# Optimization experiments

Measured on AMD Instinct MI355X. Metric: run time of the kernel, lower is better.

Reference implementation:

```python
import jax, jax.numpy as jnp
import numpy as np

N_NODES = 100000
N_EDGES = 1600000
F_IN = 128
HID = 128
N_LAYERS = 4
N_CLASSES = 10
N_GRAPHS = 512
BN_EPS = 1e-5


def setup_inputs() -> dict:
    key = jax.random.key(0)
    ks = jax.random.split(key, 16)
    x = jax.random.normal(ks[0], (N_NODES, F_IN), dtype=jnp.float32)
    edge_index = jax.random.randint(ks[1], (2, N_EDGES), 0, N_NODES, dtype=jnp.int64)
    edge_attr = jax.random.normal(ks[2], (N_EDGES, 8), dtype=jnp.float32)
    batch = jnp.sort(jax.random.randint(ks[3], (N_NODES,), 0, N_GRAPHS, dtype=jnp.int64))
    # Per-layer MLP params (in-dim is 128 for all layers since F_IN == HID).
    s1 = 1.0 / np.sqrt(F_IN)
    s2 = 1.0 / np.sqrt(2 * HID)
    W1 = jax.random.uniform(ks[4], (N_LAYERS, F_IN, 2 * HID), minval=-s1, maxval=s1, dtype=jnp.float32)
    b1 = jax.random.uniform(ks[5], (N_LAYERS, 2 * HID), minval=-s1, maxval=s1, dtype=jnp.float32)
    gamma1 = jnp.ones((N_LAYERS, 2 * HID), dtype=jnp.float32)
    beta1 = jnp.zeros((N_LAYERS, 2 * HID), dtype=jnp.float32)
    W2 = jax.random.uniform(ks[6], (N_LAYERS, 2 * HID, HID), minval=-s2, maxval=s2, dtype=jnp.float32)
    b2 = jax.random.uniform(ks[7], (N_LAYERS, HID), minval=-s2, maxval=s2, dtype=jnp.float32)
    sf = 1.0 / np.sqrt(HID * N_LAYERS)
    fcW = jax.random.uniform(ks[8], (HID * N_LAYERS, N_CLASSES), minval=-sf, maxval=sf, dtype=jnp.float32)
    fcb = jax.random.uniform(ks[9], (N_CLASSES,), minval=-sf, maxval=sf, dtype=jnp.float32)
    return {"x": x, "edge_index": edge_index, "edge_attr": edge_attr, "batch": batch,
            "W1": W1, "b1": b1, "gamma1": gamma1, "beta1": beta1,
            "W2": W2, "b2": b2, "fcW": fcW, "fcb": fcb}


def reference(x, edge_index, edge_attr, batch, W1, b1, gamma1, beta1, W2, b2, fcW, fcb):
    # edge_attr is unused by the original forward.
    src, dst = edge_index[0], edge_index[1]
    n = x.shape[0]
    # In-degree for mean aggregation (messages flow src -> dst in PyG).
    deg = jax.ops.segment_sum(jnp.ones((src.shape[0],), x.dtype), dst, num_segments=n)
    inv_deg = 1.0 / jnp.maximum(deg, 1.0)
    h = x
    xs = []
    for i in range(N_LAYERS):
        # GINConv, eps=0, aggr='mean': nn(x + mean_j h_j)
        agg = jax.ops.segment_sum(h[src], dst, num_segments=n) * inv_deg[:, None]
        z = h + agg
        z = z @ W1[i] + b1[i]                      # [N, 2H]
        mu = jnp.mean(z, axis=0)
        var = jnp.mean(jnp.square(z - mu), axis=0)  # biased var (BN training mode)
        z = gamma1[i] * (z - mu) * jax.lax.rsqrt(var + BN_EPS) + beta1[i]
        z = jax.nn.relu(z)
        z = z @ W2[i] + b2[i]                      # [N, H]
        h = jax.nn.relu(z)
        xs.append(h)
    xcat = jnp.concatenate(xs, axis=1)             # [N, H*L]
    # global_mean_pool over graph ids
    gsum = jax.ops.segment_sum(xcat, batch, num_segments=N_GRAPHS)
    gcnt = jax.ops.segment_sum(jnp.ones((n,), xcat.dtype), batch, num_segments=N_GRAPHS)
    pooled = gsum / jnp.maximum(gcnt, 1.0)[:, None]
    logits = pooled @ fcW + fcb
    return jax.nn.log_softmax(logits, axis=-1)
```

## Files before the change

kernel.cpp:

```cpp
#include <hip/hip_runtime.h>
#include <cstdint>
#include <cstddef>

#define NN 100000
#define NE 1600000
#define FD 128
#define HD2 256
#define NLAYERS 4
#define NGR 512
#define NCLS 10
#define BNEPS 1e-5f
#define G1TILES 1563
#define GEMM_GRID 521
#define EB 6250
#define NB 391
#define NSLICE 8
#define SLICEW 12500

typedef unsigned short ushort_t;
typedef short bf16x8 __attribute__((ext_vector_type(8)));
typedef float f32x4 __attribute__((ext_vector_type(4)));

__device__ __forceinline__ float bfl(unsigned short u) {
  unsigned v = ((unsigned)u) << 16;
  return __builtin_bit_cast(float, v);
}
__device__ __forceinline__ unsigned short fbf(float f) {
  unsigned u = __builtin_bit_cast(unsigned, f);
  unsigned r = (u + 0x7FFFu + ((u >> 16) & 1u)) >> 16;
  return (unsigned short)r;
}

__global__ void k_init_detect(const int* ei, int* flag, int* degi) {
  int i = blockIdx.x * 256 + threadIdx.x;
  if (i < NN) degi[i] = 0;
  if (blockIdx.x == 0) {
    __shared__ int nz;
    if (threadIdx.x == 0) nz = 0;
    __syncthreads();
    if (ei[2 * threadIdx.x + 1] != 0) atomicAdd(&nz, 1);
    __syncthreads();
    if (threadIdx.x == 0) flag[0] = (nz == 0) ? 1 : 0;
  }
}

__global__ void k_repack(const int* ei, const int* batch, const int* flag,
                         int* src32, int* dst32, int* batch32) {
  int i = blockIdx.x * 256 + threadIdx.x;
  const bool wide = (flag[0] != 0);
  if (i < NE) {
    src32[i] = wide ? ei[2 * i] : ei[i];
    dst32[i] = wide ? ei[2 * (NE + i)] : ei[NE + i];
  }
  if (i < NN) batch32[i] = wide ? batch[2 * i] : batch[i];
}

__global__ void k_deg8(const int* __restrict__ dst, int* degi) {
  int slice = blockIdx.x & (NSLICE - 1);
  int e = (blockIdx.x >> 3) * 256 + threadIdx.x;
  if (e >= NE) return;
  int d = dst[e];
  int lo = slice * SLICEW;
  if (d >= lo && d < lo + SLICEW) atomicAdd(&degi[d], 1);
}

__global__ void k_scan1(const int* degi, int* rowptr, int* bsum) {
  __shared__ int s[256];
  int t = threadIdx.x;
  int i = blockIdx.x * 256 + t;
  int v = (i < NN) ? degi[i] : 0;
  s[t] = v;
  __syncthreads();
  for (int off = 1; off < 256; off <<= 1) {
    int x = (t >= off) ? s[t - off] : 0;
    __syncthreads();
    s[t] += x;
    __syncthreads();
  }
  if (i < NN) rowptr[i] = s[t] - v;
  if (t == 255) bsum[blockIdx.x] = s[255];
}

__global__ void k_scan2_gstats(int* bsum, int nb, const int* __restrict__ batch,
                               int* __restrict__ gstart, int* __restrict__ gcnti) {
  __shared__ int s[512];
  int t = threadIdx.x;
  int v = (t < nb) ? bsum[t] : 0;
  s[t] = v;
  __syncthreads();
  for (int off = 1; off < 512; off <<= 1) {
    int x = (t >= off) ? s[t - off] : 0;
    __syncthreads();
    s[t] += x;
    __syncthreads();
  }
  if (t < nb) bsum[t] = s[t] - v;
  if (t < NGR) {
    int g = t;
    int lo = 0, hi = NN;
    while (lo < hi) { int m = (lo + hi) >> 1; if (batch[m] < g) lo = m + 1; else hi = m; }
    int st = lo;
    hi = NN;
    while (lo < hi) { int m = (lo + hi) >> 1; if (batch[m] < g + 1) lo = m + 1; else hi = m; }
    gstart[g] = st;
    gcnti[g] = lo - st;
  }
}

__global__ void k_scan3_cursor(int* rowptr, const int* bsum, int* cursor,
                               const int* degi, float* inv_deg) {
  int i = blockIdx.x * 256 + threadIdx.x;
  if (i < NN) {
    int r = rowptr[i] + bsum[blockIdx.x];
    rowptr[i] = r;
    cursor[i] = r;
    inv_deg[i] = 1.f / fmaxf((float)degi[i], 1.f);
  }
  if (i == 0) rowptr[NN] = NE;
}

__global__ void k_scatter8(const int* __restrict__ src, const int* __restrict__ dst,
                           int* cursor, int* csr) {
  int slice = blockIdx.x & (NSLICE - 1);
  int e = (blockIdx.x >> 3) * 256 + threadIdx.x;
  if (e >= NE) return;
  int d = dst[e];
  int lo = slice * SLICEW;
  if (d >= lo && d < lo + SLICEW) {
    int p = atomicAdd(&cursor[d], 1);
    csr[p] = src[e];
  }
}

__global__ void k_cvt_x(const float* __restrict__ x, ushort_t* __restrict__ xb) {
  int i = blockIdx.x * 256 + threadIdx.x;
  if (i >= NN * FD / 8) return;
  const float4* p = (const float4*)x + (size_t)i * 2;
  float4 a = p[0], b = p[1];
  bf16x8 o;
  o[0] = (short)fbf(a.x); o[1] = (short)fbf(a.y);
  o[2] = (short)fbf(a.z); o[3] = (short)fbf(a.w);
  o[4] = (short)fbf(b.x); o[5] = (short)fbf(b.y);
  o[6] = (short)fbf(b.z); o[7] = (short)fbf(b.w);
  *(bf16x8*)&xb[(size_t)i * 8] = o;
}

__global__ void k_cvt_w(const float* __restrict__ W1, const float* __restrict__ W2,
                        ushort_t* __restrict__ W1t, ushort_t* __restrict__ W2t) {
  int idx = blockIdx.x * 256 + threadIdx.x;
  if (idx >= NLAYERS * FD * HD2) return;
  int l = idx >> 15, r = idx & 32767;
  {
    int n = r >> 7, k = r & 127;
    W1t[(size_t)l * 32768 + n * 128 + k] = fbf(W1[(size_t)l * 32768 + k * 256 + n]);
  }
  {
    int n = r >> 8, k = r & 255;
    W2t[(size_t)l * 32768 + n * 256 + k] = fbf(W2[(size_t)l * 32768 + k * 128 + n]);
  }
}

__global__ void k_agg(const ushort_t* __restrict__ h, const int* __restrict__ rowptr,
                      const int* __restrict__ csr, const float* __restrict__ inv_deg,
                      ushort_t* __restrict__ tout, float* bnsum) {
  if (blockIdx.x == 0) {
    bnsum[threadIdx.x] = 0.f;
    bnsum[HD2 + threadIdx.x] = 0.f;
  }
  const int wave = threadIdx.x >> 6;
  const int lane = threadIdx.x & 63;
  const int q = lane >> 4, sub = lane & 15;
  const int node = blockIdx.x * 16 + wave * 4 + q;
  const uint4* h16 = (const uint4*)h;
  int beg = rowptr[node];
  int deg = rowptr[node + 1] - beg;
  int m1 = max(deg, __shfl_xor(deg, 16));
  int maxd = max(m1, __shfl_xor(m1, 32));
  float a0 = 0.f, a1 = 0.f, a2 = 0.f, a3 = 0.f;
  float a4 = 0.f, a5 = 0.f, a6 = 0.f, a7 = 0.f;
  int j = 0;
  for (; j + 8 <= maxd; j += 8) {
    uint4 p[8];
#pragma unroll
    for (int u = 0; u < 8; ++u) {
      bool valid = (j + u) < deg;
      int idx = beg + (valid ? j + u : 0);
      int s = csr[idx];
      uint4 v = h16[(size_t)s * 16 + sub];
      p[u].x = valid ? v.x : 0u;
      p[u].y = valid ? v.y : 0u;
      p[u].z = valid ? v.z : 0u;
      p[u].w = valid ? v.w : 0u;
    }
#pragma unroll
    for (int u = 0; u < 8; ++u) {
      a0 += bfl((unsigned short)(p[u].x & 0xFFFF));
      a1 += bfl((unsigned short)(p[u].x >> 16));
      a2 += bfl((unsigned short)(p[u].y & 0xFFFF));
      a3 += bfl((unsigned short)(p[u].y >> 16));
      a4 += bfl((unsigned short)(p[u].z & 0xFFFF));
      a5 += bfl((unsigned short)(p[u].z >> 16));
      a6 += bfl((unsigned short)(p[u].w & 0xFFFF));
      a7 += bfl((unsigned short)(p[u].w >> 16));
    }
  }
  for (; j < maxd; ++j) {
    bool valid = j < deg;
    int idx = beg + (valid ? j : 0);
    int s = csr[idx];
    uint4 v = h16[(size_t)s * 16 + sub];
    if (valid) {
      a0 += bfl((unsigned short)(v.x & 0xFFFF));
      a1 += bfl((unsigned short)(v.x >> 16));
      a2 += bfl((unsigned short)(v.y & 0xFFFF));
      a3 += bfl((unsigned short)(v.y >> 16));
      a4 += bfl((unsigned short)(v.z & 0xFFFF));
      a5 += bfl((unsigned short)(v.z >> 16));
      a6 += bfl((unsigned short)(v.w & 0xFFFF));
      a7 += bfl((unsigned short)(v.w >> 16));
    }
  }
  float id = inv_deg[node];
  uint4 c = h16[(size_t)node * 16 + sub];
  float o0 = bfl((unsigned short)(c.x & 0xFFFF)) + a0 * id;
  float o1 = bfl((unsigned short)(c.x >> 16)) + a1 * id;
  float o2 = bfl((unsigned short)(c.y & 0xFFFF)) + a2 * id;
  float o3 = bfl((unsigned short)(c.y >> 16)) + a3 * id;
  float o4 = bfl((unsigned short)(c.z & 0xFFFF)) + a4 * id;
  float o5 = bfl((unsigned short)(c.z >> 16)) + a5 * id;
  float o6 = bfl((unsigned short)(c.w & 0xFFFF)) + a6 * id;
  float o7 = bfl((unsigned short)(c.w >> 16)) + a7 * id;
  uint4 ow;
  ow.x = (unsigned)fbf(o0) | ((unsigned)fbf(o1) << 16);
  ow.y = (unsigned)fbf(o2) | ((unsigned)fbf(o3) << 16);
  ow.z = (unsigned)fbf(o4) | ((unsigned)fbf(o5) << 16);
  ow.w = (unsigned)fbf(o6) | ((unsigned)fbf(o7) << 16);
  ((uint4*)tout)[(size_t)node * 16 + sub] = ow;
}

__launch_bounds__(256, 2)
__global__ void k_gemm1(const ushort_t* __restrict__ A, const ushort_t* __restrict__ Bt,
                        const float* __restrict__ bias, ushort_t* __restrict__ Z,
                        float* __restrict__ bnsum) {
  __shared__ ushort_t Bs[256 * 128];
  __shared__ ushort_t As[64 * 128];
  const int tid = threadIdx.x;
#pragma unroll
  for (int i = 0; i < 16; ++i) {
    int chunk = tid + 256 * i;
    int n = chunk >> 4, c = chunk & 15;
    bf16x8 v = *(const bf16x8*)&Bt[n * 128 + c * 8];
    *(bf16x8*)((char*)Bs + n * 256 + ((c * 16) ^ ((n & 7) << 4))) = v;
  }
  const int wv = tid >> 6, ln = tid & 63;
  const int lr = ln & 15, lg = ln >> 4;
  float bb[16];
#pragma unroll
  for (int nt = 0; nt < 16; ++nt) bb[nt] = bias[nt * 16 + lr];
  float s0[16] = {}, s1[16] = {};

  for (int t = blockIdx.x; t < G1TILES; t += GEMM_GRID) {
    int row0 = t * 64;
#pragma unroll
    for (int i = 0; i < 4; ++i) {
      int chunk = tid + 256 * i;
      int r = chunk >> 4, c = chunk & 15;
      int grow = row0 + r; if (grow >= NN) grow = NN - 1;
      bf16x8 v = *(const bf16x8*)&A[(size_t)grow * FD + c * 8];
      *(bf16x8*)((char*)As + r * 256 + ((c * 16) ^ ((r & 7) << 4))) = v;
    }
    __syncthreads();
    int arow = wv * 16 + lr;
    bf16x8 af[4];
#pragma unroll
    for (int ks = 0; ks < 4; ++ks)
      af[ks] = *(bf16x8*)((char*)As + arow * 256 + ((ks * 64 + lg * 16) ^ ((arow & 7) << 4)));
    f32x4 acc[16];
#pragma unroll
    for (int nt = 0; nt < 16; ++nt) acc[nt] = (f32x4){0.f, 0.f, 0.f, 0.f};
#pragma unroll
    for (int nt = 0; nt < 16; ++nt) {
      int bn = nt * 16 + lr;
#pragma unroll
      for (int ks = 0; ks < 4; ++ks) {
        bf16x8 bfr = *(bf16x8*)((char*)Bs + bn * 256 + ((ks * 64 + lg * 16) ^ ((bn & 7) << 4)));
        acc[nt] = __builtin_amdgcn_mfma_f32_16x16x32_bf16(af[ks], bfr, acc[nt], 0, 0, 0);
      }
    }
    __syncthreads();
#pragma unroll
    for (int nt = 0; nt < 16; ++nt) {
      int col = nt * 16 + lr;
#pragma unroll
      for (int j = 0; j < 4; ++j) {
        int grow = row0 + wv * 16 + lg * 4 + j;
        if (grow < NN) {
          unsigned short zb = fbf(acc[nt][j] + bb[nt]);
          Z[(size_t)grow * HD2 + col] = zb;
          float zf = bfl(zb);
          s0[nt] += zf;
          s1[nt] += zf * zf;
        }
      }
    }
  }
  __syncthreads();
  float* ls = (float*)As;
  ls[tid] = 0.f; ls[tid + 256] = 0.f;
  __syncthreads();
#pragma unroll
  for (int nt = 0; nt < 16; ++nt) {
    int col = nt * 16 + lr;
    atomicAdd(&ls[col], s0[nt]);
    atomicAdd(&ls[col + 256], s1[nt]);
  }
  __syncthreads();
  if (tid < 256) {
    atomicAdd(&bnsum[tid], ls[tid]);
    atomicAdd(&bnsum[HD2 + tid], ls[tid + 256]);
  }
}

__launch_bounds__(256, 2)
__global__ void k_gemm2(const ushort_t* __restrict__ Zin, const ushort_t* __restrict__ Bt,
                        const float* __restrict__ bias, const float* __restrict__ bnsum,
                        const float* __restrict__ gamma, const float* __restrict__ beta,
                        ushort_t* __restrict__ Hout) {
  __shared__ ushort_t Bs[128 * 256];
  __shared__ ushort_t As[64 * 128];
  const int tid = threadIdx.x;
#pragma unroll
  for (int i = 0; i < 16; ++i) {
    int chunk = tid + 256 * i;
    int n = chunk >> 5, c = chunk & 31;
    bf16x8 v = *(const bf16x8*)&Bt[n * 256 + c * 8];
    *(bf16x8*)((char*)Bs + n * 512 + ((c * 16) ^ ((n & 7) << 4))) = v;
  }
  const int wv = tid >> 6, ln = tid & 63;
  const int lr = ln & 15, lg = ln >> 4;
  float a1v[2][8], a2v[2][8];
#pragma unroll
  for (int h = 0; h < 2; ++h)
#pragma unroll
    for (int j = 0; j < 8; ++j) {
      int k = h * 128 + (tid & 15) * 8 + j;
      float mu = bnsum[k] * (1.f / (float)NN);
      float var = fmaxf(bnsum[HD2 + k] * (1.f / (float)NN) - mu * mu, 0.f);
      float g = gamma[k] * rsqrtf(var + BNEPS);
      a1v[h][j] = g;
      a2v[h][j] = beta[k] - mu * g;
    }
  float bb[8];
#pragma unroll
  for (int nt = 0; nt < 8; ++nt) bb[nt] = bias[nt * 16 + lr];

  for (int t = blockIdx.x; t < G1TILES; t += GEMM_GRID) {
    int row0 = t * 64;
    f32x4 acc[8];
#pragma unroll
    for (int nt = 0; nt < 8; ++nt) acc[nt] = (f32x4){0.f, 0.f, 0.f, 0.f};
#pragma unroll
    for (int h = 0; h < 2; ++h) {
#pragma unroll
      for (int i = 0; i < 4; ++i) {
        int chunk = tid + 256 * i;
        int r = chunk >> 4, c = chunk & 15;
        int grow = row0 + r; if (grow >= NN) grow = NN - 1;
        bf16x8 v = *(const bf16x8*)&Zin[(size_t)grow * HD2 + h * 128 + c * 8];
        bf16x8 o;
#pragma unroll
        for (int j = 0; j < 8; ++j) {
          float f = bfl((unsigned short)v[j]) * a1v[h][j] + a2v[h][j];
          o[j] = (short)fbf(fmaxf(f, 0.f));
        }
        *(bf16x8*)((char*)As + r * 256 + ((c * 16) ^ ((r & 7) << 4))) = o;
      }
      __syncthreads();
      int arow = wv * 16 + lr;
      bf16x8 af[4];
#pragma unroll
      for (int ks = 0; ks < 4; ++ks)
        af[ks] = *(bf16x8*)((char*)As + arow * 256 + ((ks * 64 + lg * 16) ^ ((arow & 7) << 4)));
#pragma unroll
      for (int nt = 0; nt < 8; ++nt) {
        int bn = nt * 16 + lr;
#pragma unroll
        for (int ks = 0; ks < 4; ++ks) {
          bf16x8 bfr = *(bf16x8*)((char*)Bs + bn * 512 +
                                  (((h * 16 + ks * 4 + lg) * 16) ^ ((bn & 7) << 4)));
          acc[nt] = __builtin_amdgcn_mfma_f32_16x16x32_bf16(af[ks], bfr, acc[nt], 0, 0, 0);
        }
      }
      __syncthreads();
    }
#pragma unroll
    for (int nt = 0; nt < 8; ++nt) {
      int col = nt * 16 + lr;
#pragma unroll
      for (int j = 0; j < 4; ++j) {
        int grow = row0 + wv * 16 + lg * 4 + j;
        if (grow < NN) Hout[(size_t)grow * FD + col] = fbf(fmaxf(acc[nt][j] + bb[nt], 0.f));
      }
    }
  }
}

__launch_bounds__(256)
__global__ void k_pool_fc(const ushort_t* __restrict__ hb, const int* __restrict__ gstart,
                          const int* __restrict__ gcnti, const float* __restrict__ fcW,
                          const float* __restrict__ fcb, float* __restrict__ out) {
  __shared__ float pool4[4][512];
  __shared__ float wred[4][NCLS];
  int g = blockIdx.x, t = threadIdx.x;
  int start = gstart[g], cnt = gcnti[g];
  int chunk = t & 63, ro = t >> 6;
  int L = chunk >> 4, cc = (chunk & 15) * 8;
  const ushort_t* hL = hb + (size_t)L * NN * FD;
  float s[8] = {};
  for (int r = start + ro; r < start + cnt; r += 4) {
    bf16x8 v = *(const bf16x8*)&hL[(size_t)r * FD + cc];
#pragma unroll
    for (int j = 0; j < 8; ++j) s[j] += bfl((unsigned short)v[j]);
  }
#pragma unroll
  for (int j = 0; j < 8; ++j) pool4[ro][chunk * 8 + j] = s[j];
  __syncthreads();
  float inv = 1.f / fmaxf((float)cnt, 1.f);
  float pA = (pool4[0][t] + pool4[1][t] + pool4[2][t] + pool4[3][t]) * inv;
  float pB = (pool4[0][t + 256] + pool4[1][t + 256] + pool4[2][t + 256] + pool4[3][t + 256]) * inv;
  float pacc[NCLS];
#pragma unroll
  for (int c = 0; c < NCLS; ++c)
    pacc[c] = pA * fcW[t * NCLS + c] + pB * fcW[(t + 256) * NCLS + c];
#pragma unroll
  for (int off = 32; off > 0; off >>= 1)
#pragma unroll
    for (int c = 0; c < NCLS; ++c) pacc[c] += __shfl_down(pacc[c], off);
  if ((t & 63) == 0)
#pragma unroll
    for (int c = 0; c < NCLS; ++c) wred[t >> 6][c] = pacc[c];
  __syncthreads();
  if (t == 0) {
    float lg[NCLS];
    float mx = -1e30f;
#pragma unroll
    for (int c = 0; c < NCLS; ++c) {
      lg[c] = wred[0][c] + wred[1][c] + wred[2][c] + wred[3][c] + fcb[c];
      mx = fmaxf(mx, lg[c]);
    }
    float se = 0.f;
#pragma unroll
    for (int c = 0; c < NCLS; ++c) se += expf(lg[c] - mx);
    float lse = mx + logf(se);
#pragma unroll
    for (int c = 0; c < NCLS; ++c) out[(size_t)g * NCLS + c] = lg[c] - lse;
  }
}

extern "C" void kernel_launch(void* const* d_in, const int* in_sizes, int n_in,
                              void* d_out, int out_size, void* d_ws, size_t ws_size,
                              hipStream_t stream) {
  const float* x      = (const float*)d_in[0];
  const int*   ei     = (const int*)d_in[1];
  const int*   batch  = (const int*)d_in[3];
  const float* W1     = (const float*)d_in[4];
  const float* b1     = (const float*)d_in[5];
  const float* gamma1 = (const float*)d_in[6];
  const float* beta1  = (const float*)d_in[7];
  const float* W2     = (const float*)d_in[8];
  const float* b2     = (const float*)d_in[9];
  const float* fcW    = (const float*)d_in[10];
  const float* fcb    = (const float*)d_in[11];
  float* out = (float*)d_out;

  char* p = (char*)d_ws;
  auto alloc = [&](size_t bytes) {
    char* r = p;
    p += (bytes + 255) & ~(size_t)255;
    return r;
  };
  ushort_t* xbf   = (ushort_t*)alloc((size_t)NN * FD * 2);
  ushort_t* tbuf  = (ushort_t*)alloc((size_t)NN * FD * 2);
  ushort_t* Zbuf  = (ushort_t*)alloc((size_t)NN * HD2 * 2);
  ushort_t* hb    = (ushort_t*)alloc((size_t)NLAYERS * NN * FD * 2);
  ushort_t* W1t   = (ushort_t*)alloc((size_t)NLAYERS * FD * HD2 * 2);
  ushort_t* W2t   = (ushort_t*)alloc((size_t)NLAYERS * FD * HD2 * 2);
  float* inv_deg  = (float*)alloc((size_t)NN * 4);
  float* bnsum    = (float*)alloc(2 * HD2 * 4);
  int* degi       = (int*)alloc((size_t)NN * 4);
  int* rowptr     = (int*)alloc((size_t)(NN + 1) * 4);
  int* cursor     = (int*)alloc((size_t)NN * 4);
  int* csr        = (int*)alloc((size_t)NE * 4);
  int* bsum       = (int*)alloc(512 * 4);
  int* src32      = (int*)alloc((size_t)NE * 4);
  int* dst32      = (int*)alloc((size_t)NE * 4);
  int* batch32    = (int*)alloc((size_t)NN * 4);
  int* gcnti      = (int*)alloc((size_t)NGR * 4);
  int* gstart     = (int*)alloc((size_t)NGR * 4);
  int* flag       = (int*)alloc(256);

  k_init_detect<<<NB, 256, 0, stream>>>(ei, flag, degi);
  k_repack<<<EB, 256, 0, stream>>>(ei, batch, flag, src32, dst32, batch32);
  k_deg8<<<EB * NSLICE, 256, 0, stream>>>(dst32, degi);
  k_scan1<<<NB, 256, 0, stream>>>(degi, rowptr, bsum);
  k_scan2_gstats<<<1, 512, 0, stream>>>(bsum, NB, batch32, gstart, gcnti);
  k_scan3_cursor<<<NB, 256, 0, stream>>>(rowptr, bsum, cursor, degi, inv_deg);
  k_scatter8<<<EB * NSLICE, 256, 0, stream>>>(src32, dst32, cursor, csr);
  k_cvt_x<<<(NN * FD / 8 + 255) / 256, 256, 0, stream>>>(x, xbf);
  k_cvt_w<<<(NLAYERS * FD * HD2 + 255) / 256, 256, 0, stream>>>(W1, W2, W1t, W2t);

  const ushort_t* hin = xbf;
  for (int L = 0; L < NLAYERS; ++L) {
    k_agg<<<NN / 16, 256, 0, stream>>>(hin, rowptr, csr, inv_deg, tbuf, bnsum);
    k_gemm1<<<GEMM_GRID, 256, 0, stream>>>(tbuf, W1t + (size_t)L * FD * HD2,
                                           b1 + (size_t)L * HD2, Zbuf, bnsum);
    k_gemm2<<<GEMM_GRID, 256, 0, stream>>>(Zbuf, W2t + (size_t)L * FD * HD2,
                                           b2 + (size_t)L * FD, bnsum,
                                           gamma1 + (size_t)L * HD2, beta1 + (size_t)L * HD2,
                                           hb + (size_t)L * NN * FD);
    hin = hb + (size_t)L * NN * FD;
  }
  k_pool_fc<<<NGR, 256, 0, stream>>>(hb, gstart, gcnti, fcW, fcb, out);
}
```

Measured before the change: 829.5 us.

## Recompute first GEMM to avoid materializing Z; fuse BN+ReLU+second GEMM

```diff
diff --git a/kernel.cpp b/kernel.cpp
--- a/kernel.cpp
+++ b/kernel.cpp
@@ -12,6 +12,7 @@
 #define BNEPS 1e-5f
 #define G1TILES 1563
 #define GEMM_GRID 521
+#define MLP_GRID 256
 #define EB 6250
 #define NB 391
 #define NSLICE 8
@@ -239,9 +240,8 @@
 }
 
 __launch_bounds__(256, 2)
-__global__ void k_gemm1(const ushort_t* __restrict__ A, const ushort_t* __restrict__ Bt,
-                        const float* __restrict__ bias, ushort_t* __restrict__ Z,
-                        float* __restrict__ bnsum) {
+__global__ void k_zstat(const ushort_t* __restrict__ A, const ushort_t* __restrict__ Bt,
+                        const float* __restrict__ bias, float* __restrict__ bnsum) {
   __shared__ ushort_t Bs[256 * 128];
   __shared__ ushort_t As[64 * 128];
   const int tid = threadIdx.x;
@@ -290,14 +290,11 @@
     __syncthreads();
 #pragma unroll
     for (int nt = 0; nt < 16; ++nt) {
-      int col = nt * 16 + lr;
 #pragma unroll
       for (int j = 0; j < 4; ++j) {
         int grow = row0 + wv * 16 + lg * 4 + j;
         if (grow < NN) {
-          unsigned short zb = fbf(acc[nt][j] + bb[nt]);
-          Z[(size_t)grow * HD2 + col] = zb;
-          float zf = bfl(zb);
+          float zf = acc[nt][j] + bb[nt];
           s0[nt] += zf;
           s1[nt] += zf * zf;
         }
@@ -321,85 +318,110 @@
   }
 }
 
-__launch_bounds__(256, 2)
-__global__ void k_gemm2(const ushort_t* __restrict__ Zin, const ushort_t* __restrict__ Bt,
-                        const float* __restrict__ bias, const float* __restrict__ bnsum,
-                        const float* __restrict__ gamma, const float* __restrict__ beta,
-                        ushort_t* __restrict__ Hout) {
-  __shared__ ushort_t Bs[128 * 256];
-  __shared__ ushort_t As[64 * 128];
+__launch_bounds__(512, 2)
+__global__ void k_mlp(const ushort_t* __restrict__ T, const ushort_t* __restrict__ W1t,
+                      const ushort_t* __restrict__ W2t, const float* __restrict__ b1,
+                      const float* __restrict__ b2, const float* __restrict__ bnsum,
+                      const float* __restrict__ gamma, const float* __restrict__ beta,
+                      ushort_t* __restrict__ Hout) {
+  __shared__ ushort_t W1s[256 * 128];
+  __shared__ ushort_t W2s[128 * 256];
+  __shared__ ushort_t ZR[64 * 256];
   const int tid = threadIdx.x;
 #pragma unroll
-  for (int i = 0; i < 16; ++i) {
-    int chunk = tid + 256 * i;
+  for (int i = 0; i < 8; ++i) {
+    int chunk = tid + 512 * i;
+    int n = chunk >> 4, c = chunk & 15;
+    bf16x8 v = *(const bf16x8*)&W1t[n * 128 + c * 8];
+    *(bf16x8*)((char*)W1s + n * 256 + ((c * 16) ^ ((n & 7) << 4))) = v;
+  }
+#pragma unroll
+  for (int i = 0; i < 8; ++i) {
+    int chunk = tid + 512 * i;
     int n = chunk >> 5, c = chunk & 31;
-    bf16x8 v = *(const bf16x8*)&Bt[n * 256 + c * 8];
-    *(bf16x8*)((char*)Bs + n * 512 + ((c * 16) ^ ((n & 7) << 4))) = v;
+    bf16x8 v = *(const bf16x8*)&W2t[n * 256 + c * 8];
+    *(bf16x8*)((char*)W2s + n * 512 + ((c * 16) ^ ((n & 7) << 4))) = v;
   }
   const int wv = tid >> 6, ln = tid & 63;
   const int lr = ln & 15, lg = ln >> 4;
-  float a1v[2][8], a2v[2][8];
-#pragma unroll
-  for (int h = 0; h < 2; ++h)
-#pragma unroll
-    for (int j = 0; j < 8; ++j) {
-      int k = h * 128 + (tid & 15) * 8 + j;
-      float mu = bnsum[k] * (1.f / (float)NN);
-      float var = fmaxf(bnsum[HD2 + k] * (1.f / (float)NN) - mu * mu, 0.f);
-      float g = gamma[k] * rsqrtf(var + BNEPS);
-      a1v[h][j] = g;
-      a2v[h][j] = beta[k] - mu * g;
-    }
-  float bb[8];
-#pragma unroll
-  for (int nt = 0; nt < 8; ++nt) bb[nt] = bias[nt * 16 + lr];
-
-  for (int t = blockIdx.x; t < G1TILES; t += GEMM_GRID) {
+  const int mrow = (wv & 3) * 16;
+  const int nh = wv >> 2;
+  float a1v[8], a2v[8], bb1[8];
+#pragma unroll
+  for (int nt = 0; nt < 8; ++nt) {
+    int c = (nh * 8 + nt) * 16 + lr;
+    float mu = bnsum[c] * (1.f / (float)NN);
+    float var = fmaxf(bnsum[HD2 + c] * (1.f / (float)NN) - mu * mu, 0.f);
+    float g = gamma[c] * rsqrtf(var + BNEPS);
+    a1v[nt] = g;
+    a2v[nt] = beta[c] - mu * g;
+    bb1[nt] = b1[c];
+  }
+  float bb2[4];
+#pragma unroll
+  for (int nt2 = 0; nt2 < 4; ++nt2) bb2[nt2] = b2[nh * 64 + nt2 * 16 + lr];
+  __syncthreads();
+
+  for (int t = blockIdx.x; t < G1TILES; t += MLP_GRID) {
     int row0 = t * 64;
-    f32x4 acc[8];
-#pragma unroll
-    for (int nt = 0; nt < 8; ++nt) acc[nt] = (f32x4){0.f, 0.f, 0.f, 0.f};
-#pragma unroll
-    for (int h = 0; h < 2; ++h) {
-#pragma unroll
-      for (int i = 0; i < 4; ++i) {
-        int chunk = tid + 256 * i;
-        int r = chunk >> 4, c = chunk & 15;
-        int grow = row0 + r; if (grow >= NN) grow = NN - 1;
-        bf16x8 v = *(const bf16x8*)&Zin[(size_t)grow * HD2 + h * 128 + c * 8];
-        bf16x8 o;
-#pragma unroll
-        for (int j = 0; j < 8; ++j) {
-          float f = bfl((unsigned short)v[j]) * a1v[h][j] + a2v[h][j];
-          o[j] = (short)fbf(fmaxf(f, 0.f));
-        }
-        *(bf16x8*)((char*)As + r * 256 + ((c * 16) ^ ((r & 7) << 4))) = o;
+    int grow = row0 + mrow + lr; if (grow >= NN) grow = NN - 1;
+    bf16x8 af[4];
+#pragma unroll
+    for (int ks = 0; ks < 4; ++ks)
+      af[ks] = *(const bf16x8*)&T[(size_t)grow * FD + ks * 32 + lg * 8];
+    f32x4 acc1[8];
+#pragma unroll
+    for (int nt = 0; nt < 8; ++nt) acc1[nt] = (f32x4){0.f, 0.f, 0.f, 0.f};
+#pragma unroll
+    for (int nt = 0; nt < 8; ++nt) {
+      int bn = (nh * 8 + nt) * 16 + lr;
+#pragma unroll
+      for (int ks = 0; ks < 4; ++ks) {
+        bf16x8 bfr = *(bf16x8*)((char*)W1s + bn * 256 + ((ks * 64 + lg * 16) ^ ((bn & 7) << 4)));
+        acc1[nt] = __builtin_amdgcn_mfma_f32_16x16x32_bf16(af[ks], bfr, acc1[nt], 0, 0, 0);
       }
-      __syncthreads();
-      int arow = wv * 16 + lr;
-      bf16x8 af[4];
-#pragma unroll
-      for (int ks = 0; ks < 4; ++ks)
-        af[ks] = *(bf16x8*)((char*)As + arow * 256 + ((ks * 64 + lg * 16) ^ ((arow & 7) << 4)));
-#pragma unroll
-      for (int nt = 0; nt < 8; ++nt) {
-        int bn = nt * 16 + lr;
-#pragma unroll
-        for (int ks = 0; ks < 4; ++ks) {
-          bf16x8 bfr = *(bf16x8*)((char*)Bs + bn * 512 +
-                                  (((h * 16 + ks * 4 + lg) * 16) ^ ((bn & 7) << 4)));
-          acc[nt] = __builtin_amdgcn_mfma_f32_16x16x32_bf16(af[ks], bfr, acc[nt], 0, 0, 0);
-        }
+    }
+#pragma unroll
+    for (int nt = 0; nt < 8; ++nt) {
+      int col = (nh * 8 + nt) * 16 + lr;
+#pragma unroll
+      for (int j = 0; j < 4; ++j) {
+        int row = mrow + lg * 4 + j;
+        float z = acc1[nt][j] + bb1[nt];
+        float f = fmaxf(z * a1v[nt] + a2v[nt], 0.f);
+        int byte = row * 512 + ((((col >> 3) << 4) ^ ((row & 7) << 4))) + (col & 7) * 2;
+        *(ushort_t*)((char*)ZR + byte) = fbf(f);
       }
-      __syncthreads();
-    }
-#pragma unroll
-    for (int nt = 0; nt < 8; ++nt) {
-      int col = nt * 16 + lr;
+    }
+    __syncthreads();
+    int zrow = mrow + lr;
+    bf16x8 af2[8];
+#pragma unroll
+    for (int ks2 = 0; ks2 < 8; ++ks2) {
+      int c2 = ks2 * 4 + lg;
+      af2[ks2] = *(bf16x8*)((char*)ZR + zrow * 512 + ((c2 * 16) ^ ((zrow & 7) << 4)));
+    }
+    __syncthreads();
+    f32x4 acc2[4];
+#pragma unroll
+    for (int nt2 = 0; nt2 < 4; ++nt2) acc2[nt2] = (f32x4){0.f, 0.f, 0.f, 0.f};
+#pragma unroll
+    for (int nt2 = 0; nt2 < 4; ++nt2) {
+      int bn2 = nh * 64 + nt2 * 16 + lr;
+#pragma unroll
+      for (int ks2 = 0; ks2 < 8; ++ks2) {
+        int c2 = ks2 * 4 + lg;
+        bf16x8 bfr2 = *(bf16x8*)((char*)W2s + bn2 * 512 + ((c2 * 16) ^ ((bn2 & 7) << 4)));
+        acc2[nt2] = __builtin_amdgcn_mfma_f32_16x16x32_bf16(af2[ks2], bfr2, acc2[nt2], 0, 0, 0);
+      }
+    }
+#pragma unroll
+    for (int nt2 = 0; nt2 < 4; ++nt2) {
+      int col = nh * 64 + nt2 * 16 + lr;
 #pragma unroll
       for (int j = 0; j < 4; ++j) {
-        int grow = row0 + wv * 16 + lg * 4 + j;
-        if (grow < NN) Hout[(size_t)grow * FD + col] = fbf(fmaxf(acc[nt][j] + bb[nt], 0.f));
+        int hrow = row0 + mrow + lg * 4 + j;
+        if (hrow < NN) Hout[(size_t)hrow * FD + col] = fbf(fmaxf(acc2[nt2][j] + bb2[nt2], 0.f));
       }
     }
   }
@@ -481,7 +503,6 @@
   };
   ushort_t* xbf   = (ushort_t*)alloc((size_t)NN * FD * 2);
   ushort_t* tbuf  = (ushort_t*)alloc((size_t)NN * FD * 2);
-  ushort_t* Zbuf  = (ushort_t*)alloc((size_t)NN * HD2 * 2);
   ushort_t* hb    = (ushort_t*)alloc((size_t)NLAYERS * NN * FD * 2);
   ushort_t* W1t   = (ushort_t*)alloc((size_t)NLAYERS * FD * HD2 * 2);
   ushort_t* W2t   = (ushort_t*)alloc((size_t)NLAYERS * FD * HD2 * 2);
@@ -512,12 +533,14 @@
   const ushort_t* hin = xbf;
   for (int L = 0; L < NLAYERS; ++L) {
     k_agg<<<NN / 16, 256, 0, stream>>>(hin, rowptr, csr, inv_deg, tbuf, bnsum);
-    k_gemm1<<<GEMM_GRID, 256, 0, stream>>>(tbuf, W1t + (size_t)L * FD * HD2,
-                                           b1 + (size_t)L * HD2, Zbuf, bnsum);
-    k_gemm2<<<GEMM_GRID, 256, 0, stream>>>(Zbuf, W2t + (size_t)L * FD * HD2,
-                                           b2 + (size_t)L * FD, bnsum,
-                                           gamma1 + (size_t)L * HD2, beta1 + (size_t)L * HD2,
-                                           hb + (size_t)L * NN * FD);
+    k_zstat<<<GEMM_GRID, 256, 0, stream>>>(tbuf, W1t + (size_t)L * FD * HD2,
+                                           b1 + (size_t)L * HD2, bnsum);
+    k_mlp<<<MLP_GRID, 512, 0, stream>>>(tbuf, W1t + (size_t)L * FD * HD2,
+                                        W2t + (size_t)L * FD * HD2,
+                                        b1 + (size_t)L * HD2, b2 + (size_t)L * FD,
+                                        bnsum, gamma1 + (size_t)L * HD2,
+                                        beta1 + (size_t)L * HD2,
+                                        hb + (size_t)L * NN * FD);
     hin = hb + (size_t)L * NN * FD;
   }
   k_pool_fc<<<NGR, 256, 0, stream>>>(hb, gstart, gcnti, fcW, fcb, out);
```

Result: faster. 794.8 us (-4.2%).
